# Optimization experiments

Hardware: AMD Instinct MI355X
Metric: run time of the kernel (lower is better)

Reference implementation:

```python
import jax, jax.numpy as jnp
import numpy as np

PIDS = (0, 1, 2, 3)
BIG = 1e9  # sentinel for masked-out pairwise distances


def setup_inputs() -> dict:
    key = jax.random.key(0)
    k1, k2, k3, k4 = jax.random.split(key, 4)
    B, N, D = 512, 256, 4
    return {
        "target": jax.random.normal(k1, (B, N, D), dtype=jnp.float32),
        "reco": jax.random.normal(k2, (B, N, D), dtype=jnp.float32),
        "in_pid": jax.random.randint(k3, (B, N), 0, 4, dtype=jnp.int64),
        "out_pid": jax.random.randint(k4, (B, N), 0, 4, dtype=jnp.int64),
    }


def _chamfer_split_pid(target, reco, in_pid, out_pid):
    B = target.shape[0]
    dt = target.dtype
    # squared norms and cross term -> pairwise Euclidean distances [B, N, M]
    x2 = jnp.sum(target * target, axis=-1)          # [B, N]
    y2 = jnp.sum(reco * reco, axis=-1)              # [B, M]
    xy = jnp.einsum("bnd,bmd->bnm", target, reco)   # [B, N, M]
    dist2 = x2[:, :, None] + y2[:, None, :] - 2.0 * xy
    dist = jnp.sqrt(jnp.maximum(dist2, 0.0))        # [B, N, M]
    norm_x = jnp.sqrt(x2)                            # [B, N]
    norm_y = jnp.sqrt(y2)                            # [B, M]

    per_pid_losses = []
    for pid in PIDS[1:]:
        mx = in_pid == pid                           # [B, N]
        my = out_pid == pid                          # [B, M]
        cx = jnp.sum(mx, axis=-1)                    # [B]
        cy = jnp.sum(my, axis=-1)                    # [B]
        n_in = jnp.maximum(cx, 1).astype(dt)
        n_out = jnp.maximum(cy, 1).astype(dt)
        pair_mask = mx[:, :, None] & my[:, None, :]
        dmask = jnp.where(pair_mask, dist, BIG)
        min_xy = jnp.min(dmask, axis=-1)             # per-x min over masked y, [B, N]
        min_yx = jnp.min(dmask, axis=-2)             # per-y min over masked x, [B, M]
        sum_min_xy = jnp.sum(jnp.where(mx, min_xy, 0.0), axis=-1)
        sum_min_yx = jnp.sum(jnp.where(my, min_yx, 0.0), axis=-1)
        both = 0.5 * (sum_min_xy / n_out + sum_min_yx / n_in)
        only_x = jnp.sum(jnp.where(mx, norm_x, 0.0), axis=-1) / n_in
        only_y = jnp.sum(jnp.where(my, norm_y, 0.0), axis=-1) / n_out
        loss_p = jnp.where(cy == 0, only_x, jnp.where(cx == 0, only_y, both))
        per_pid_losses.append(loss_p)

    nonzero_per_batch = jnp.sum(jnp.stack(per_pid_losses, axis=0), axis=0)  # [B]

    my0 = out_pid == 0
    c0 = jnp.maximum(jnp.sum(my0, axis=-1), 1).astype(dt)
    zero_per_batch = jnp.sum(jnp.where(my0, norm_y, 0.0), axis=-1) / c0    # [B]

    # reduction == 'mean'
    return jnp.sum(nonzero_per_batch) / B, zero_per_batch / B


def reference(target, reco, in_pid, out_pid):
    return _chamfer_split_pid(target, reco, in_pid, out_pid)
```

## Files before the change

### kernel.cpp

```cpp
#include <hip/hip_runtime.h>
#include <math.h>


constexpr int BATCH = 512;
constexpr int NP    = 256;
constexpr float INF2 = 1e30f;

__device__ __forceinline__ float dist2_f4(const float4 a, const float4 b) {
    const float dx = a.x - b.x;
    const float dy = a.y - b.y;
    const float dz = a.z - b.z;
    const float dw = a.w - b.w;
    return dx * dx + dy * dy + dz * dz + dw * dw;
}

__device__ __forceinline__ float min_scan(const float4 xp, const float4* seg, int cnt) {
    float m0 = INF2, m1 = INF2, m2 = INF2, m3 = INF2;
    int j = 0;
    for (; j + 4 <= cnt; j += 4) {
        const float4 A = seg[j], B = seg[j + 1], C = seg[j + 2], D = seg[j + 3];
        m0 = fminf(m0, dist2_f4(xp, A));
        m1 = fminf(m1, dist2_f4(xp, B));
        m2 = fminf(m2, dist2_f4(xp, C));
        m3 = fminf(m3, dist2_f4(xp, D));
    }
    for (; j < cnt; ++j) m0 = fminf(m0, dist2_f4(xp, seg[j]));
    return fminf(fminf(m0, m1), fminf(m2, m3));
}

__global__ __launch_bounds__(512) void chamfer_pid_kernel(
    const float* __restrict__ target,
    const float* __restrict__ reco,
    const int*   __restrict__ in_pid,
    const int*   __restrict__ out_pid,
    float* __restrict__ out,
    float* __restrict__ ws)
{
    const int b    = blockIdx.x;
    const int tid  = threadIdx.x;
    const int k    = tid & (NP - 1);
    const int half = tid >> 8;

    __shared__ float4 sxs[NP], sys[NP];
    __shared__ int   s_cx[4], s_cy[4], s_offx[4], s_offy[4];
    __shared__ float s_sxy[4], s_syx[4], s_snx[4], s_sny[4];

    if (tid < 4) {
        s_cx[tid] = 0;    s_cy[tid] = 0;
        s_sxy[tid] = 0.f; s_syx[tid] = 0.f;
        s_snx[tid] = 0.f; s_sny[tid] = 0.f;
    }
    __syncthreads();

    float4 pt;
    int pid, slot;
    if (half == 0) {
        pt  = reinterpret_cast<const float4*>(target)[(size_t)b * NP + k];
        pid = in_pid[(size_t)b * NP + k];
        slot = atomicAdd(&s_cx[pid], 1);
    } else {
        pt  = reinterpret_cast<const float4*>(reco)[(size_t)b * NP + k];
        pid = out_pid[(size_t)b * NP + k];
        slot = atomicAdd(&s_cy[pid], 1);
    }
    __syncthreads();

    if (tid == 0) {
        int ox = 0, oy = 0;
        #pragma unroll
        for (int q = 0; q < 4; ++q) {
            s_offx[q] = ox; ox += s_cx[q];
            s_offy[q] = oy; oy += s_cy[q];
        }
    }
    __syncthreads();

    if (half == 0) sxs[s_offx[pid] + slot] = pt;
    else           sys[s_offy[pid] + slot] = pt;
    __syncthreads();

    if (half == 0) {
        const int p = (k >= s_offx[1]) + (k >= s_offx[2]) + (k >= s_offx[3]);
        const float4 xp = sxs[k];
        if (p >= 1) {
            const float nrm = sqrtf(xp.x * xp.x + xp.y * xp.y + xp.z * xp.z + xp.w * xp.w);
            atomicAdd(&s_snx[p], nrm);
            const int cnt = s_cy[p];
            if (cnt > 0) {
                const float mn = min_scan(xp, (const float4*)&sys[s_offy[p]], cnt);
                atomicAdd(&s_sxy[p], sqrtf(mn));
            }
        }
    } else {
        const int p = (k >= s_offy[1]) + (k >= s_offy[2]) + (k >= s_offy[3]);
        const float4 yp = sys[k];
        const float nrm = sqrtf(yp.x * yp.x + yp.y * yp.y + yp.z * yp.z + yp.w * yp.w);
        atomicAdd(&s_sny[p], nrm);
        if (p >= 1) {
            const int cnt = s_cx[p];
            if (cnt > 0) {
                const float mn = min_scan(yp, (const float4*)&sxs[s_offx[p]], cnt);
                atomicAdd(&s_syx[p], sqrtf(mn));
            }
        }
    }
    __syncthreads();

    if (tid == 0) {
        float nonzero = 0.0f;
        #pragma unroll
        for (int q = 1; q < 4; ++q) {
            const int cxq = s_cx[q];
            const int cyq = s_cy[q];
            const float n_in  = (float)(cxq > 1 ? cxq : 1);
            const float n_out = (float)(cyq > 1 ? cyq : 1);
            float loss;
            if (cyq == 0) {
                loss = s_snx[q] / n_in;
            } else if (cxq == 0) {
                loss = s_sny[q] / n_out;
            } else {
                loss = 0.5f * (s_sxy[q] / n_out + s_syx[q] / n_in);
            }
            nonzero += loss;
        }
        ws[b] = nonzero;

        const int c0 = s_cy[0];
        const float c0f = (float)(c0 > 1 ? c0 : 1);
        out[1 + b] = (s_sny[0] / c0f) / (float)BATCH;
    }
}

__global__ __launch_bounds__(256) void chamfer_reduce_kernel(
    const float* __restrict__ ws,
    float* __restrict__ out)
{
    __shared__ float red[256];
    const int i = threadIdx.x;
    red[i] = ws[i] + ws[i + 256];
    __syncthreads();
    #pragma unroll
    for (int s = 128; s > 0; s >>= 1) {
        if (i < s) red[i] += red[i + s];
        __syncthreads();
    }
    if (i == 0) {
        out[0] = red[0] / (float)BATCH;
    }
}

extern "C" void kernel_launch(void* const* d_in, const int* in_sizes, int n_in,
                              void* d_out, int out_size, void* d_ws, size_t ws_size,
                              hipStream_t stream) {
    const float* target  = (const float*)d_in[0];
    const float* reco    = (const float*)d_in[1];
    const int*   in_pid  = (const int*)d_in[2];
    const int*   out_pid = (const int*)d_in[3];
    float* out = (float*)d_out;
    float* ws  = (float*)d_ws;

    chamfer_pid_kernel<<<BATCH, 512, 0, stream>>>(target, reco, in_pid, out_pid, out, ws);
    chamfer_reduce_kernel<<<1, 256, 0, stream>>>(ws, out);
}
```

Before: 16.71 us.

## Split each batch across two blocks by direction and halve inner scan range

Launches two blocks per batch element: one computes the target-to-reco nearest-neighbour term and the other the reco-to-target term. Within a block, both halves of the threads scan half of the opposite segment each, and the partial minima are merged through shared memory. The goal is shorter per-thread scans and more blocks to fill the GPU. The cost is that each block redundantly reloads the inputs and redoes the pid bucketing. The final reduction is also rewritten to use wavefront shuffles over 1024 partial values.

```diff
diff --git a/kernel.cpp b/kernel.cpp
--- a/kernel.cpp
+++ b/kernel.cpp
@@ -14,21 +14,22 @@
     return dx * dx + dy * dy + dz * dz + dw * dw;
 }
 
-__device__ __forceinline__ float min_scan(const float4 xp, const float4* seg, int cnt) {
+__device__ __forceinline__ float min_scan_range(const float4 xp, const float4* seg,
+                                                int lo, int hi) {
     float m0 = INF2, m1 = INF2, m2 = INF2, m3 = INF2;
-    int j = 0;
-    for (; j + 4 <= cnt; j += 4) {
+    int j = lo;
+    for (; j + 4 <= hi; j += 4) {
         const float4 A = seg[j], B = seg[j + 1], C = seg[j + 2], D = seg[j + 3];
         m0 = fminf(m0, dist2_f4(xp, A));
         m1 = fminf(m1, dist2_f4(xp, B));
         m2 = fminf(m2, dist2_f4(xp, C));
         m3 = fminf(m3, dist2_f4(xp, D));
     }
-    for (; j < cnt; ++j) m0 = fminf(m0, dist2_f4(xp, seg[j]));
+    for (; j < hi; ++j) m0 = fminf(m0, dist2_f4(xp, seg[j]));
     return fminf(fminf(m0, m1), fminf(m2, m3));
 }
 
-__global__ __launch_bounds__(512) void chamfer_pid_kernel(
+__global__ __launch_bounds__(512, 8) void chamfer_pid_kernel(
     const float* __restrict__ target,
     const float* __restrict__ reco,
     const int*   __restrict__ in_pid,
@@ -36,19 +37,22 @@
     float* __restrict__ out,
     float* __restrict__ ws)
 {
-    const int b    = blockIdx.x;
+    const int bp   = blockIdx.x;
+    const int b    = bp >> 1;
+    const int role = bp & 1;
     const int tid  = threadIdx.x;
     const int k    = tid & (NP - 1);
     const int half = tid >> 8;
 
     __shared__ float4 sxs[NP], sys[NP];
     __shared__ int   s_cx[4], s_cy[4], s_offx[4], s_offy[4];
-    __shared__ float s_sxy[4], s_syx[4], s_snx[4], s_sny[4];
+    __shared__ float s_sA[4];
+    __shared__ float s_sN[4];
+    __shared__ float s_half[NP];
 
     if (tid < 4) {
-        s_cx[tid] = 0;    s_cy[tid] = 0;
-        s_sxy[tid] = 0.f; s_syx[tid] = 0.f;
-        s_snx[tid] = 0.f; s_sny[tid] = 0.f;
+        s_cx[tid] = 0;   s_cy[tid] = 0;
+        s_sA[tid] = 0.f; s_sN[tid] = 0.f;
     }
     __syncthreads();
 
@@ -79,56 +83,64 @@
     else           sys[s_offy[pid] + slot] = pt;
     __syncthreads();
 
-    if (half == 0) {
-        const int p = (k >= s_offx[1]) + (k >= s_offx[2]) + (k >= s_offx[3]);
-        const float4 xp = sxs[k];
-        if (p >= 1) {
-            const float nrm = sqrtf(xp.x * xp.x + xp.y * xp.y + xp.z * xp.z + xp.w * xp.w);
-            atomicAdd(&s_snx[p], nrm);
-            const int cnt = s_cy[p];
-            if (cnt > 0) {
-                const float mn = min_scan(xp, (const float4*)&sys[s_offy[p]], cnt);
-                atomicAdd(&s_sxy[p], sqrtf(mn));
-            }
-        }
-    } else {
-        const int p = (k >= s_offy[1]) + (k >= s_offy[2]) + (k >= s_offy[3]);
-        const float4 yp = sys[k];
-        const float nrm = sqrtf(yp.x * yp.x + yp.y * yp.y + yp.z * yp.z + yp.w * yp.w);
-        atomicAdd(&s_sny[p], nrm);
-        if (p >= 1) {
-            const int cnt = s_cx[p];
-            if (cnt > 0) {
-                const float mn = min_scan(yp, (const float4*)&sxs[s_offx[p]], cnt);
-                atomicAdd(&s_syx[p], sqrtf(mn));
-            }
+    const float4* own    = (role == 0) ? sxs : sys;
+    const float4* opp    = (role == 0) ? sys : sxs;
+    const int*    ownOff = (role == 0) ? s_offx : s_offy;
+    const int*    oppOff = (role == 0) ? s_offy : s_offx;
+    const int*    oppCnt = (role == 0) ? s_cy : s_cx;
+
+    const int p = (k >= ownOff[1]) + (k >= ownOff[2]) + (k >= ownOff[3]);
+    const float4 q4 = own[k];
+    const int cnt = oppCnt[p];
+
+    float mn = INF2;
+    if (p >= 1 && cnt > 0) {
+        const int h  = (cnt + 1) >> 1;
+        const int lo = half ? h : 0;
+        const int hi = half ? cnt : h;
+        mn = min_scan_range(q4, opp + oppOff[p], lo, hi);
+    }
+    if (half) s_half[k] = mn;
+    __syncthreads();
+
+    if (!half) {
+        const float nrm = sqrtf(q4.x * q4.x + q4.y * q4.y + q4.z * q4.z + q4.w * q4.w);
+        atomicAdd(&s_sN[p], nrm);
+        if (p >= 1 && cnt > 0) {
+            mn = fminf(mn, s_half[k]);
+            atomicAdd(&s_sA[p], sqrtf(mn));
         }
     }
     __syncthreads();
 
     if (tid == 0) {
-        float nonzero = 0.0f;
-        #pragma unroll
-        for (int q = 1; q < 4; ++q) {
-            const int cxq = s_cx[q];
-            const int cyq = s_cy[q];
-            const float n_in  = (float)(cxq > 1 ? cxq : 1);
-            const float n_out = (float)(cyq > 1 ? cyq : 1);
-            float loss;
-            if (cyq == 0) {
-                loss = s_snx[q] / n_in;
-            } else if (cxq == 0) {
-                loss = s_sny[q] / n_out;
-            } else {
-                loss = 0.5f * (s_sxy[q] / n_out + s_syx[q] / n_in);
+        float contrib = 0.0f;
+        if (role == 0) {
+            #pragma unroll
+            for (int q = 1; q < 4; ++q) {
+                const int cxq = s_cx[q], cyq = s_cy[q];
+                if (cyq == 0)
+                    contrib += s_sN[q] / (float)(cxq > 1 ? cxq : 1);
+                else if (cxq > 0)
+                    contrib += 0.5f * s_sA[q] / (float)(cyq > 1 ? cyq : 1);
             }
-            nonzero += loss;
+            ws[2 * b] = contrib;
+        } else {
+            #pragma unroll
+            for (int q = 1; q < 4; ++q) {
+                const int cxq = s_cx[q], cyq = s_cy[q];
+                if (cyq > 0) {
+                    if (cxq == 0)
+                        contrib += s_sN[q] / (float)(cyq > 1 ? cyq : 1);
+                    else
+                        contrib += 0.5f * s_sA[q] / (float)(cxq > 1 ? cxq : 1);
+                }
+            }
+            ws[2 * b + 1] = contrib;
+
+            const int c0 = s_cy[0];
+            out[1 + b] = (s_sN[0] / (float)(c0 > 1 ? c0 : 1)) / (float)BATCH;
         }
-        ws[b] = nonzero;
-
-        const int c0 = s_cy[0];
-        const float c0f = (float)(c0 > 1 ? c0 : 1);
-        out[1 + b] = (s_sny[0] / c0f) / (float)BATCH;
     }
 }
 
@@ -136,17 +148,17 @@
     const float* __restrict__ ws,
     float* __restrict__ out)
 {
-    __shared__ float red[256];
+    __shared__ float red[4];
     const int i = threadIdx.x;
-    red[i] = ws[i] + ws[i + 256];
+    const float4 v = reinterpret_cast<const float4*>(ws)[i];
+    float s = (v.x + v.y) + (v.z + v.w);
+    #pragma unroll
+    for (int off = 32; off > 0; off >>= 1)
+        s += __shfl_xor(s, off, 64);
+    if ((i & 63) == 0) red[i >> 6] = s;
     __syncthreads();
-    #pragma unroll
-    for (int s = 128; s > 0; s >>= 1) {
-        if (i < s) red[i] += red[i + s];
-        __syncthreads();
-    }
     if (i == 0) {
-        out[0] = red[0] / (float)BATCH;
+        out[0] = ((red[0] + red[1]) + (red[2] + red[3])) / (float)BATCH;
     }
 }
 
@@ -160,6 +172,6 @@
     float* out = (float*)d_out;
     float* ws  = (float*)d_ws;
 
-    chamfer_pid_kernel<<<BATCH, 512, 0, stream>>>(target, reco, in_pid, out_pid, out, ws);
+    chamfer_pid_kernel<<<2 * BATCH, 512, 0, stream>>>(target, reco, in_pid, out_pid, out, ws);
     chamfer_reduce_kernel<<<1, 256, 0, stream>>>(ws, out);
 }
```

Result: slower. 17.36 us (+3.9%).
